# Performance work log

Measured on AMD Instinct MI355X. Metric: run time of the kernel, lower is better.

The kernel has to match this reference:

```python
import jax, jax.numpy as jnp
import numpy as np

EPS = 1e-6      # torch F.pairwise_distance default eps (added to the difference)
MARGIN = 1.0

def _cdist_eps(a, b):
    # Exact ||a_i - b_j + eps||_2 via expansion:
    # ||a-b+eps||^2 = ||a||^2 + ||b||^2 - 2 a.b + 2*eps*(sum(a)-sum(b)) + D*eps^2
    D = a.shape[-1]
    sq = (jnp.sum(a * a, axis=1)[:, None]
          + jnp.sum(b * b, axis=1)[None, :]
          - 2.0 * (a @ b.T)
          + 2.0 * EPS * (jnp.sum(a, axis=1)[:, None] - jnp.sum(b, axis=1)[None, :])
          + D * EPS * EPS)
    return jnp.sqrt(jnp.maximum(sq, 0.0))

def setup_inputs() -> dict:
    key = jax.random.key(0)
    k1, k2, k3 = jax.random.split(key, 3)
    B, D = 4096, 1024
    return {
        'anchor_embeddings': jax.random.normal(k1, (B, D), dtype=jnp.float32),
        'positive_embeddings': jax.random.normal(k2, (B, D), dtype=jnp.float32),
        'negative_embeddings': jax.random.normal(k3, (B, D), dtype=jnp.float32),
    }

def reference(anchor_embeddings, positive_embeddings, negative_embeddings):
    a, p, n = anchor_embeddings, positive_embeddings, negative_embeddings
    # per-row anchor-positive and anchor-negative distances
    d_ap = jnp.linalg.norm(a - p + EPS, axis=-1)          # [B]
    d_an_row = jnp.linalg.norm(a - n + EPS, axis=-1)      # [B]

    # hardest negative: for each anchor, max over negatives with dist < d_ap[i], else 0
    dan_mat = _cdist_eps(a, n)                            # [B, B]
    mask_n = dan_mat < d_ap[:, None]
    hard_n = jnp.where(mask_n.any(axis=1),
                       jnp.max(jnp.where(mask_n, dan_mat, -jnp.inf), axis=1),
                       0.0)
    d_an = jnp.mean(hard_n)                               # scalar

    # hardest positive: for each anchor, min over positives with dist > d(a_i, n_i), else 0
    dpp_mat = _cdist_eps(a, p)                            # [B, B]
    mask_p = dpp_mat > d_an_row[:, None]
    hard_p = jnp.where(mask_p.any(axis=1),
                       jnp.min(jnp.where(mask_p, dpp_mat, jnp.inf), axis=1),
                       0.0)
    d_pp = jnp.mean(hard_p)                               # scalar

    loss = jnp.mean(jnp.clip(d_ap - 0.5 * d_pp - 0.5 * d_an + MARGIN, 0.0, None))
    return loss
```

## Files before the change

kernel.cpp:

```cpp
#include <hip/hip_runtime.h>


#define NB 4096
#define DIM 1024
#define EPSF 1e-6f
#define D_EPS2 (1024.0f * 1e-6f * 1e-6f)

#define BM 128
#define BK 64

typedef __bf16  bf16x8 __attribute__((ext_vector_type(8)));
typedef float   f32x4  __attribute__((ext_vector_type(4)));

__device__ __forceinline__ unsigned short f2bf(float x) {
    unsigned u = __float_as_uint(x);
    u += 0x7FFFu + ((u >> 16) & 1u);
    return (unsigned short)(u >> 16);
}

__device__ __forceinline__ void g2l16(const unsigned short* g, unsigned short* l) {
    __builtin_amdgcn_global_load_lds(
        (const __attribute__((address_space(1))) unsigned int*)g,
        (__attribute__((address_space(3))) unsigned int*)l, 16, 0, 0);
}


__global__ __launch_bounds__(256) void row_stats_kernel(
    const float* __restrict__ a, const float* __restrict__ p,
    const float* __restrict__ n,
    unsigned short* __restrict__ abf, unsigned short* __restrict__ pbf,
    unsigned short* __restrict__ nbf, float* __restrict__ stats)
{
    const int t    = threadIdx.x;
    const int wave = t >> 6, lane = t & 63;
    const int row  = blockIdx.x * 4 + wave;
    const size_t base = (size_t)row * DIM;

    const float4* a4 = (const float4*)(a + base);
    const float4* p4 = (const float4*)(p + base);
    const float4* n4 = (const float4*)(n + base);

    float v[8] = {0,0,0,0,0,0,0,0};
#pragma unroll
    for (int c = 0; c < 4; c++) {
        const int idx = c * 64 + lane;
        const float4 va = a4[idx];
        const float4 vp = p4[idx];
        const float4 vn = n4[idx];
        const float fa[4] = {va.x, va.y, va.z, va.w};
        const float fp[4] = {vp.x, vp.y, vp.z, vp.w};
        const float fn[4] = {vn.x, vn.y, vn.z, vn.w};
#pragma unroll
        for (int e = 0; e < 4; e++) {
            v[0] += fa[e];           v[1] += fa[e] * fa[e];
            v[2] += fp[e];           v[3] += fp[e] * fp[e];
            v[4] += fn[e];           v[5] += fn[e] * fn[e];
            float dp = fa[e] - fp[e] + EPSF;  v[6] += dp * dp;
            float dn = fa[e] - fn[e] + EPSF;  v[7] += dn * dn;
        }
        ushort4 ba, bp, bn;
        ba.x = f2bf(fa[0]); ba.y = f2bf(fa[1]); ba.z = f2bf(fa[2]); ba.w = f2bf(fa[3]);
        bp.x = f2bf(fp[0]); bp.y = f2bf(fp[1]); bp.z = f2bf(fp[2]); bp.w = f2bf(fp[3]);
        bn.x = f2bf(fn[0]); bn.y = f2bf(fn[1]); bn.z = f2bf(fn[2]); bn.w = f2bf(fn[3]);
        ((ushort4*)(abf + base))[idx] = ba;
        ((ushort4*)(pbf + base))[idx] = bp;
        ((ushort4*)(nbf + base))[idx] = bn;
    }

#pragma unroll
    for (int m = 32; m >= 1; m >>= 1)
#pragma unroll
        for (int q = 0; q < 8; q++) v[q] += __shfl_xor(v[q], m);

    if (lane == 0) {
        stats[0 * NB + row] = v[1] + 2.0f * EPSF * v[0] + D_EPS2;
        stats[1 * NB + row] = v[5] - 2.0f * EPSF * v[4];
        stats[2 * NB + row] = v[3] - 2.0f * EPSF * v[2];
        stats[3 * NB + row] = sqrtf(v[6]);
        stats[4 * NB + row] = sqrtf(v[7]);
        ((unsigned*)stats)[5 * NB + row] = 0u;
        ((unsigned*)stats)[6 * NB + row] = 0x7f800000u;
    }
}

__global__ __launch_bounds__(256, 2) void gemm_mask_kernel(
    const unsigned short* __restrict__ Abf,
    const unsigned short* __restrict__ Nbf,
    const unsigned short* __restrict__ Pbf,
    float* __restrict__ stats)
{
    const int i0 = blockIdx.x * BM;
    const int j0 = blockIdx.y * BM;

    __shared__ unsigned short sA[BM * BK];
    __shared__ unsigned short sN[BM * BK];
    __shared__ unsigned short sP[BM * BK];

    const int t    = threadIdx.x;
    const int wave = t >> 6, lane = t & 63;
    const int wm   = wave >> 1, wn = wave & 1;
    const int quad = lane >> 4, lrow = lane & 15;

    const int srow = lane >> 3;
    const int kch  = ((lane & 7) ^ srow) * 8;
    const unsigned short* gA = Abf + (size_t)(i0 + wave * 32 + srow) * DIM + kch;
    const unsigned short* gN = Nbf + (size_t)(j0 + wave * 32 + srow) * DIM + kch;
    const unsigned short* gP = Pbf + (size_t)(j0 + wave * 32 + srow) * DIM + kch;
    unsigned short* lA = sA + (wave * 32) * BK;
    unsigned short* lN = sN + (wave * 32) * BK;
    unsigned short* lP = sP + (wave * 32) * BK;

    const int rsw0 = ((0 * 4 + quad) ^ (lrow & 7)) * 8;
    const int rsw1 = ((1 * 4 + quad) ^ (lrow & 7)) * 8;
    const unsigned short* pa  = sA + (wm * 64 + lrow) * BK;
    const unsigned short* pbn = sN + (wn * 64 + lrow) * BK;
    const unsigned short* pbp = sP + (wn * 64 + lrow) * BK;

    f32x4 accN[4][4], accP[4][4];
#pragma unroll
    for (int im = 0; im < 4; im++)
#pragma unroll
        for (int jn = 0; jn < 4; jn++) {
            accN[im][jn] = (f32x4)(0.0f);
            accP[im][jn] = (f32x4)(0.0f);
        }

    for (int kt = 0; kt < DIM; kt += BK) {
        __syncthreads();
#pragma unroll
        for (int g = 0; g < 4; g++) {
            g2l16(gA + (size_t)kt + g * 8 * DIM, lA + g * 8 * BK);
            g2l16(gN + (size_t)kt + g * 8 * DIM, lN + g * 8 * BK);
            g2l16(gP + (size_t)kt + g * 8 * DIM, lP + g * 8 * BK);
        }
        __syncthreads();

#pragma unroll
        for (int half = 0; half < 2; half++) {
            const int rsw = half ? rsw1 : rsw0;
            bf16x8 afr[4], bn_fr[4], bp_fr[4];
#pragma unroll
            for (int im = 0; im < 4; im++)
                afr[im] = *(const bf16x8*)(pa + im * 16 * BK + rsw);
#pragma unroll
            for (int jn = 0; jn < 4; jn++) {
                bn_fr[jn] = *(const bf16x8*)(pbn + jn * 16 * BK + rsw);
                bp_fr[jn] = *(const bf16x8*)(pbp + jn * 16 * BK + rsw);
            }
#pragma unroll
            for (int im = 0; im < 4; im++)
#pragma unroll
                for (int jn = 0; jn < 4; jn++) {
                    accN[im][jn] = __builtin_amdgcn_mfma_f32_16x16x32_bf16(
                        afr[im], bn_fr[jn], accN[im][jn], 0, 0, 0);
                    accP[im][jn] = __builtin_amdgcn_mfma_f32_16x16x32_bf16(
                        afr[im], bp_fr[jn], accP[im][jn], 0, 0, 0);
                }
        }
    }

    const float* __restrict__ base_a = stats + 0 * NB;
    const float* __restrict__ cn_v   = stats + 1 * NB;
    const float* __restrict__ cp_v   = stats + 2 * NB;
    const float* __restrict__ d_ap   = stats + 3 * NB;
    const float* __restrict__ d_an   = stats + 4 * NB;
    unsigned* __restrict__ hard_n = ((unsigned*)stats) + 5 * NB;
    unsigned* __restrict__ hard_p = ((unsigned*)stats) + 6 * NB;

#pragma unroll
    for (int im = 0; im < 4; im++) {
#pragma unroll
        for (int r = 0; r < 4; r++) {
            const int gi = i0 + wm * 64 + im * 16 + quad * 4 + r;
            const float cutN = d_ap[gi];
            const float cutP = d_an[gi];
            const float bi   = base_a[gi];
            float bestN = 0.0f;
            float bestP = __uint_as_float(0x7f800000u);
#pragma unroll
            for (int jn = 0; jn < 4; jn++) {
                const int gj = j0 + wn * 64 + jn * 16 + lrow;
                const float dN = sqrtf(fmaxf(bi + cn_v[gj] - 2.0f * accN[im][jn][r], 0.0f));
                const float dP = sqrtf(fmaxf(bi + cp_v[gj] - 2.0f * accP[im][jn][r], 0.0f));
                if (dN < cutN && dN > bestN) bestN = dN;
                if (dP > cutP && dP < bestP) bestP = dP;
            }
#pragma unroll
            for (int m = 1; m < 16; m <<= 1) {
                bestN = fmaxf(bestN, __shfl_xor(bestN, m));
                bestP = fminf(bestP, __shfl_xor(bestP, m));
            }
            if (lrow == 0) {
                const unsigned bn_ = __float_as_uint(bestN);
                const unsigned bp_ = __float_as_uint(bestP);
                if (bn_ != 0u)          atomicMax(hard_n + gi, bn_);
                if (bp_ != 0x7f800000u) atomicMin(hard_p + gi, bp_);
            }
        }
    }
}

__global__ __launch_bounds__(1024) void finalize_kernel(
    const float* __restrict__ stats, float* __restrict__ out)
{
    const unsigned* hard_n = ((const unsigned*)stats) + 5 * NB;
    const unsigned* hard_p = ((const unsigned*)stats) + 6 * NB;
    const float*    d_ap   = stats + 3 * NB;
    const int t = threadIdx.x;
    const int wave = t >> 6, lane = t & 63;
    __shared__ float pn[16], pp[16];
    __shared__ float s_dan, s_dpp;

    float sn = 0.0f, sp = 0.0f;
    for (int i = t; i < NB; i += 1024) {
        sn += __uint_as_float(hard_n[i]);
        const unsigned hp = hard_p[i];
        if (hp != 0x7f800000u) sp += __uint_as_float(hp);
    }
#pragma unroll
    for (int m = 32; m >= 1; m >>= 1) {
        sn += __shfl_xor(sn, m);
        sp += __shfl_xor(sp, m);
    }
    if (lane == 0) { pn[wave] = sn; pp[wave] = sp; }
    __syncthreads();
    if (t == 0) {
        float an = 0.0f, ap = 0.0f;
#pragma unroll
        for (int w = 0; w < 16; w++) { an += pn[w]; ap += pp[w]; }
        s_dan = an / (float)NB;
        s_dpp = ap / (float)NB;
    }
    __syncthreads();
    const float dan = s_dan, dpp = s_dpp;

    float accv = 0.0f;
    for (int i = t; i < NB; i += 1024)
        accv += fmaxf(d_ap[i] - 0.5f * dpp - 0.5f * dan + 1.0f, 0.0f);
#pragma unroll
    for (int m = 32; m >= 1; m >>= 1) accv += __shfl_xor(accv, m);
    if (lane == 0) pn[wave] = accv;
    __syncthreads();
    if (t == 0) {
        float s = 0.0f;
#pragma unroll
        for (int w = 0; w < 16; w++) s += pn[w];
        out[0] = s / (float)NB;
    }
}

extern "C" void kernel_launch(void* const* d_in, const int* in_sizes, int n_in,
                              void* d_out, int out_size, void* d_ws, size_t ws_size,
                              hipStream_t stream) {
    const float* a = (const float*)d_in[0];
    const float* p = (const float*)d_in[1];
    const float* n = (const float*)d_in[2];
    float* out = (float*)d_out;

    unsigned short* abf = (unsigned short*)d_ws;
    unsigned short* pbf = abf + (size_t)NB * DIM;
    unsigned short* nbf = pbf + (size_t)NB * DIM;
    float* stats = (float*)(nbf + (size_t)NB * DIM);

    row_stats_kernel<<<NB / 4, 256, 0, stream>>>(a, p, n, abf, pbf, nbf, stats);

    dim3 grid(NB / BM, NB / BM);
    gemm_mask_kernel<<<grid, 256, 0, stream>>>(abf, nbf, pbf, stats);

    finalize_kernel<<<1, 1024, 0, stream>>>(stats, out);
}
```

Baseline: 183.6 us.

## Double-buffer LDS tiles with BK=32 to overlap global loads with MFMA

Splits the K tile in half and adds two LDS buffers per operand, so the next tile's global-to-LDS copies are issued while MFMAs run on the current buffer. This leaves one barrier per stage instead of two and removes the exposed load latency. The swizzle and load mapping are reworked for the narrower tile, and the occupancy hint of 2 blocks per CU is removed from launch bounds. Risks are more K iterations, each with less compute, and possible register or occupancy changes.

```diff
diff --git a/kernel.cpp b/kernel.cpp
--- a/kernel.cpp
+++ b/kernel.cpp
@@ -7,7 +7,7 @@
 #define D_EPS2 (1024.0f * 1e-6f * 1e-6f)
 
 #define BM 128
-#define BK 64
+#define BK 32
 
 typedef __bf16  bf16x8 __attribute__((ext_vector_type(8)));
 typedef float   f32x4  __attribute__((ext_vector_type(4)));
@@ -83,7 +83,7 @@
     }
 }
 
-__global__ __launch_bounds__(256, 2) void gemm_mask_kernel(
+__global__ __launch_bounds__(256) void gemm_mask_kernel(
     const unsigned short* __restrict__ Abf,
     const unsigned short* __restrict__ Nbf,
     const unsigned short* __restrict__ Pbf,
@@ -92,29 +92,25 @@
     const int i0 = blockIdx.x * BM;
     const int j0 = blockIdx.y * BM;
 
-    __shared__ unsigned short sA[BM * BK];
-    __shared__ unsigned short sN[BM * BK];
-    __shared__ unsigned short sP[BM * BK];
+    __shared__ unsigned short sA[2][BM * BK];
+    __shared__ unsigned short sN[2][BM * BK];
+    __shared__ unsigned short sP[2][BM * BK];
 
     const int t    = threadIdx.x;
     const int wave = t >> 6, lane = t & 63;
     const int wm   = wave >> 1, wn = wave & 1;
     const int quad = lane >> 4, lrow = lane & 15;
 
-    const int srow = lane >> 3;
-    const int kch  = ((lane & 7) ^ srow) * 8;
-    const unsigned short* gA = Abf + (size_t)(i0 + wave * 32 + srow) * DIM + kch;
-    const unsigned short* gN = Nbf + (size_t)(j0 + wave * 32 + srow) * DIM + kch;
-    const unsigned short* gP = Pbf + (size_t)(j0 + wave * 32 + srow) * DIM + kch;
-    unsigned short* lA = sA + (wave * 32) * BK;
-    unsigned short* lN = sN + (wave * 32) * BK;
-    unsigned short* lP = sP + (wave * 32) * BK;
-
-    const int rsw0 = ((0 * 4 + quad) ^ (lrow & 7)) * 8;
-    const int rsw1 = ((1 * 4 + quad) ^ (lrow & 7)) * 8;
-    const unsigned short* pa  = sA + (wm * 64 + lrow) * BK;
-    const unsigned short* pbn = sN + (wn * 64 + lrow) * BK;
-    const unsigned short* pbp = sP + (wn * 64 + lrow) * BK;
+    const int srow = t >> 2;
+    const int kch  = ((t & 3) ^ ((srow >> 1) & 3)) * 8;
+    const unsigned short* gA = Abf + (size_t)(i0 + srow) * DIM + kch;
+    const unsigned short* gN = Nbf + (size_t)(j0 + srow) * DIM + kch;
+    const unsigned short* gP = Pbf + (size_t)(j0 + srow) * DIM + kch;
+    const int lwav = wave * 512;
+
+    const int rsw  = (quad ^ ((lrow >> 1) & 3)) * 8;
+    const int aoff = (wm * 64 + lrow) * BK;
+    const int boff = (wn * 64 + lrow) * BK;
 
     f32x4 accN[4][4], accP[4][4];
 #pragma unroll
@@ -125,39 +121,54 @@
             accP[im][jn] = (f32x4)(0.0f);
         }
 
-    for (int kt = 0; kt < DIM; kt += BK) {
+#define STAGE(B, KT)                                                          \
+    _Pragma("unroll")                                                         \
+    for (int g = 0; g < 2; g++) {                                             \
+        g2l16(gA + (size_t)(KT) + (size_t)(g * 64) * DIM,                     \
+              &sA[B][g * 64 * BK + lwav]);                                    \
+        g2l16(gN + (size_t)(KT) + (size_t)(g * 64) * DIM,                     \
+              &sN[B][g * 64 * BK + lwav]);                                    \
+        g2l16(gP + (size_t)(KT) + (size_t)(g * 64) * DIM,                     \
+              &sP[B][g * 64 * BK + lwav]);                                    \
+    }
+
+#define COMPUTE(B)                                                            \
+  {                                                                           \
+    bf16x8 afr[4], bn_fr[4], bp_fr[4];                                        \
+    _Pragma("unroll")                                                         \
+    for (int im = 0; im < 4; im++)                                            \
+        afr[im] = *(const bf16x8*)&sA[B][aoff + im * 16 * BK + rsw];          \
+    _Pragma("unroll")                                                         \
+    for (int jn = 0; jn < 4; jn++) {                                          \
+        bn_fr[jn] = *(const bf16x8*)&sN[B][boff + jn * 16 * BK + rsw];        \
+        bp_fr[jn] = *(const bf16x8*)&sP[B][boff + jn * 16 * BK + rsw];        \
+    }                                                                         \
+    _Pragma("unroll")                                                         \
+    for (int im = 0; im < 4; im++)                                            \
+        _Pragma("unroll")                                                     \
+        for (int jn = 0; jn < 4; jn++) {                                      \
+            accN[im][jn] = __builtin_amdgcn_mfma_f32_16x16x32_bf16(           \
+                afr[im], bn_fr[jn], accN[im][jn], 0, 0, 0);                   \
+            accP[im][jn] = __builtin_amdgcn_mfma_f32_16x16x32_bf16(           \
+                afr[im], bp_fr[jn], accP[im][jn], 0, 0, 0);                   \
+        }                                                                     \
+  }
+
+    STAGE(0, 0);
+    __syncthreads();
+
+#pragma unroll 1
+    for (int k2 = 0; k2 < 16; ++k2) {
+        STAGE(1, (2 * k2 + 1) * BK);
+        COMPUTE(0);
         __syncthreads();
-#pragma unroll
-        for (int g = 0; g < 4; g++) {
-            g2l16(gA + (size_t)kt + g * 8 * DIM, lA + g * 8 * BK);
-            g2l16(gN + (size_t)kt + g * 8 * DIM, lN + g * 8 * BK);
-            g2l16(gP + (size_t)kt + g * 8 * DIM, lP + g * 8 * BK);
-        }
+        if (k2 < 15) STAGE(0, (2 * k2 + 2) * BK);
+        COMPUTE(1);
         __syncthreads();
-
-#pragma unroll
-        for (int half = 0; half < 2; half++) {
-            const int rsw = half ? rsw1 : rsw0;
-            bf16x8 afr[4], bn_fr[4], bp_fr[4];
-#pragma unroll
-            for (int im = 0; im < 4; im++)
-                afr[im] = *(const bf16x8*)(pa + im * 16 * BK + rsw);
-#pragma unroll
-            for (int jn = 0; jn < 4; jn++) {
-                bn_fr[jn] = *(const bf16x8*)(pbn + jn * 16 * BK + rsw);
-                bp_fr[jn] = *(const bf16x8*)(pbp + jn * 16 * BK + rsw);
-            }
-#pragma unroll
-            for (int im = 0; im < 4; im++)
-#pragma unroll
-                for (int jn = 0; jn < 4; jn++) {
-                    accN[im][jn] = __builtin_amdgcn_mfma_f32_16x16x32_bf16(
-                        afr[im], bn_fr[jn], accN[im][jn], 0, 0, 0);
-                    accP[im][jn] = __builtin_amdgcn_mfma_f32_16x16x32_bf16(
-                        afr[im], bp_fr[jn], accP[im][jn], 0, 0, 0);
-                }
-        }
-    }
+    }
+
+#undef COMPUTE
+#undef STAGE
 
     const float* __restrict__ base_a = stats + 0 * NB;
     const float* __restrict__ cn_v   = stats + 1 * NB;
```

Result: slower. 268.4 us (+46.2%).
